# Kernel tuning notes

Hardware: AMD Instinct MI355X
Metric: run time of the kernel (lower is better)

The kernel has to match this reference:

```python
import jax, jax.numpy as jnp
import numpy as np

EPS = 1e-8
L_CENTER, L_ALIGN, L_MARGIN = 1.0, 0.1, 0.05
B, D = 16384, 2048


def setup_inputs() -> dict:
    key = jax.random.key(0)
    kf, kl, ks = jax.random.split(key, 3)
    feats = jax.random.normal(kf, (B, D), dtype=jnp.float32)
    feats = feats / jnp.linalg.norm(feats, axis=-1, keepdims=True)  # module assumes normalized
    labels = jax.random.randint(kl, (B,), 0, 2, dtype=jnp.int32)
    sessions = jax.random.randint(ks, (B,), 0, 2, dtype=jnp.int32)
    return {"features": feats, "labels": labels, "sessions": sessions}


def _cos(a, b):
    # F.cosine_similarity semantics: dot / max(|a||b|, eps)
    num = jnp.sum(a * b, axis=-1)
    den = jnp.maximum(jnp.linalg.norm(a, axis=-1) * jnp.linalg.norm(b, axis=-1), EPS)
    return num / den


def reference(features, labels, sessions):
    # group id: (label, session) -> 2*label + session ; centers order (0,0),(0,1),(1,0),(1,1)
    g = labels * 2 + sessions
    counts = jax.ops.segment_sum(jnp.ones((features.shape[0],), features.dtype), g, num_segments=4)
    sums = jax.ops.segment_sum(features, g, num_segments=4)  # (4, D)
    centers = sums / counts[:, None]

    # 1) center loss: mean over samples of (1 - cos(f_i, center_{g_i}))
    center_loss = jnp.mean(1.0 - _cos(features, centers[g]))

    # 2) align loss: same class, across sessions -> pairs (c00,c01), (c10,c11)
    align_loss = ((1.0 - _cos(centers[0], centers[1])) + (1.0 - _cos(centers[2], centers[3]))) / 2.0

    # 3) angular margin: cross-class center pairs (2x2 = 4 pairs), mean cosine
    c0 = centers[:2]  # class 0 centers (2, D)
    c1 = centers[2:]  # class 1 centers (2, D)
    margin_loss = jnp.mean(_cos(c0[:, None, :], c1[None, :, :]))

    total = L_CENTER * center_loss + L_ALIGN * align_loss + L_MARGIN * margin_loss
    return total, center_loss, align_loss, margin_loss
```

## Files before the change

kernel.cpp:

```cpp
#include <hip/hip_runtime.h>
#include <math.h>

constexpr int B_ROWS = 16384;
constexpr int D_COLS = 2048;
constexpr float EPS_F = 1e-8f;

constexpr int NRB = 256;
constexpr int NCS = 8;
constexpr int ROWS_PER_RB = 64;
constexpr int ROWS_PER_H = 16;

constexpr int WS_DOTS = 2048;
constexpr int WS_PART = 16384;

__global__ __launch_bounds__(256, 8) void pass1_partial_sums(
    const float* __restrict__ feat, const int* __restrict__ lab,
    const int* __restrict__ ses, float* __restrict__ ws) {
  const int t = threadIdx.x;
  const int rb = blockIdx.x >> 3;
  const int cs = blockIdx.x & 7;
  const int c = t & 63;
  const int h = t >> 6;
  const int row0 = rb * ROWS_PER_RB;

  __shared__ float4 w[ROWS_PER_RB];
  __shared__ float4 red[16 * 64];

  if (t < ROWS_PER_RB) {
    const int r = row0 + t;
    const int g = lab[r] * 2 + ses[r];
    w[t] = make_float4(g == 0 ? 1.f : 0.f, g == 1 ? 1.f : 0.f,
                       g == 2 ? 1.f : 0.f, g == 3 ? 1.f : 0.f);
  }
  __syncthreads();

  float4 a0 = {0.f, 0.f, 0.f, 0.f};
  float4 a1 = a0, a2 = a0, a3 = a0;

  const float4* fb = (const float4*)feat
      + (size_t)(row0 + h * ROWS_PER_H) * 512 + cs * 64 + c;
  #pragma unroll 4
  for (int r = 0; r < ROWS_PER_H; ++r) {
    const float4 v = fb[(size_t)r * 512];
    const float4 wr = w[h * ROWS_PER_H + r];
    a0.x += v.x * wr.x; a0.y += v.y * wr.x; a0.z += v.z * wr.x; a0.w += v.w * wr.x;
    a1.x += v.x * wr.y; a1.y += v.y * wr.y; a1.z += v.z * wr.y; a1.w += v.w * wr.y;
    a2.x += v.x * wr.z; a2.y += v.y * wr.z; a2.z += v.z * wr.z; a2.w += v.w * wr.z;
    a3.x += v.x * wr.w; a3.y += v.y * wr.w; a3.z += v.z * wr.w; a3.w += v.w * wr.w;
  }

  red[(0 * 4 + h) * 64 + c] = a0;
  red[(1 * 4 + h) * 64 + c] = a1;
  red[(2 * 4 + h) * 64 + c] = a2;
  red[(3 * 4 + h) * 64 + c] = a3;
  __syncthreads();

  {
    const int g = t >> 6;
    float4 acc = red[(g * 4 + 0) * 64 + c];
    #pragma unroll
    for (int hh = 1; hh < 4; ++hh) {
      const float4 v = red[(g * 4 + hh) * 64 + c];
      acc.x += v.x; acc.y += v.y; acc.z += v.z; acc.w += v.w;
    }
    float4* part = (float4*)(ws + WS_PART);
    part[(size_t)rb * 2048 + g * 512 + cs * 64 + c] = acc;
  }

  if (cs == 0 && t == 0) {
    float4 cnt = {0.f, 0.f, 0.f, 0.f};
    #pragma unroll
    for (int r = 0; r < ROWS_PER_RB; ++r) {
      const float4 wr = w[r];
      cnt.x += wr.x; cnt.y += wr.y; cnt.z += wr.z; cnt.w += wr.w;
    }
    ((float4*)ws)[rb] = cnt;
  }
}

__global__ __launch_bounds__(256) void pass2_reduce(float* __restrict__ ws) {
  const int t = threadIdx.x;
  const int pair = t & 15;
  const int chunk = t >> 4;
  const int g = pair >> 2;
  const int cl = pair & 3;
  const int j4 = g * 512 + blockIdx.x * 4 + cl;

  float4 s = {0.f, 0.f, 0.f, 0.f};
  const float4* part = (const float4*)(ws + WS_PART);
  for (int p = chunk; p < NRB; p += 16) {
    const float4 v = part[(size_t)p * 2048 + j4];
    s.x += v.x; s.y += v.y; s.z += v.z; s.w += v.w;
  }

  __shared__ float4 lds[256];
  lds[t] = s;
  __syncthreads();

  __shared__ float4 sg[4][4];
  if (t < 16) {
    float4 acc = lds[t];
    #pragma unroll
    for (int ch = 1; ch < 16; ++ch) {
      const float4 v = lds[ch * 16 + t];
      acc.x += v.x; acc.y += v.y; acc.z += v.z; acc.w += v.w;
    }
    sg[t >> 2][t & 3] = acc;
  }
  __syncthreads();

  if (t == 0) {
    float n0 = 0, n1 = 0, n2 = 0, n3 = 0;
    float d01 = 0, d23 = 0, d02 = 0, d03 = 0, d12 = 0, d13 = 0;
    #pragma unroll
    for (int cl2 = 0; cl2 < 4; ++cl2) {
      const float4 s0 = sg[0][cl2], s1 = sg[1][cl2];
      const float4 s2 = sg[2][cl2], s3 = sg[3][cl2];
      n0 += s0.x*s0.x + s0.y*s0.y + s0.z*s0.z + s0.w*s0.w;
      n1 += s1.x*s1.x + s1.y*s1.y + s1.z*s1.z + s1.w*s1.w;
      n2 += s2.x*s2.x + s2.y*s2.y + s2.z*s2.z + s2.w*s2.w;
      n3 += s3.x*s3.x + s3.y*s3.y + s3.z*s3.z + s3.w*s3.w;
      d01 += s0.x*s1.x + s0.y*s1.y + s0.z*s1.z + s0.w*s1.w;
      d23 += s2.x*s3.x + s2.y*s3.y + s2.z*s3.z + s2.w*s3.w;
      d02 += s0.x*s2.x + s0.y*s2.y + s0.z*s2.z + s0.w*s2.w;
      d03 += s0.x*s3.x + s0.y*s3.y + s0.z*s3.z + s0.w*s3.w;
      d12 += s1.x*s2.x + s1.y*s2.y + s1.z*s2.z + s1.w*s2.w;
      d13 += s1.x*s3.x + s1.y*s3.y + s1.z*s3.z + s1.w*s3.w;
    }
    float* dst = ws + WS_DOTS + blockIdx.x * 12;
    dst[0] = n0;  dst[1] = n1;  dst[2] = n2;  dst[3] = n3;
    dst[4] = d01; dst[5] = d23; dst[6] = d02; dst[7] = d03;
    dst[8] = d12; dst[9] = d13; dst[10] = 0.f; dst[11] = 0.f;
  }
}

__global__ __launch_bounds__(256) void pass3_finalize(
    const float* __restrict__ ws, float* __restrict__ out) {
  const int t = threadIdx.x;
  float n0 = 0, n1 = 0, n2 = 0, n3 = 0;
  float d01 = 0, d23 = 0, d02 = 0, d03 = 0, d12 = 0, d13 = 0;
  float k0 = 0, k1 = 0, k2 = 0, k3 = 0;

  if (t < 128) {
    const float* src = ws + WS_DOTS + t * 12;
    n0 = src[0]; n1 = src[1]; n2 = src[2]; n3 = src[3];
    d01 = src[4]; d23 = src[5]; d02 = src[6]; d03 = src[7];
    d12 = src[8]; d13 = src[9];
  }
  {
    const float4 cta = ((const float4*)ws)[t];
    k0 = cta.x; k1 = cta.y; k2 = cta.z; k3 = cta.w;
  }

  #pragma unroll
  for (int m = 32; m >= 1; m >>= 1) {
    n0  += __shfl_xor(n0, m, 64);  n1  += __shfl_xor(n1, m, 64);
    n2  += __shfl_xor(n2, m, 64);  n3  += __shfl_xor(n3, m, 64);
    d01 += __shfl_xor(d01, m, 64); d23 += __shfl_xor(d23, m, 64);
    d02 += __shfl_xor(d02, m, 64); d03 += __shfl_xor(d03, m, 64);
    d12 += __shfl_xor(d12, m, 64); d13 += __shfl_xor(d13, m, 64);
    k0  += __shfl_xor(k0, m, 64);  k1  += __shfl_xor(k1, m, 64);
    k2  += __shfl_xor(k2, m, 64);  k3  += __shfl_xor(k3, m, 64);
  }

  __shared__ float red[4][14];
  const int wv = t >> 6, ln = t & 63;
  if (ln == 0) {
    red[wv][0] = n0;  red[wv][1] = n1;  red[wv][2] = n2;  red[wv][3] = n3;
    red[wv][4] = d01; red[wv][5] = d23; red[wv][6] = d02; red[wv][7] = d03;
    red[wv][8] = d12; red[wv][9] = d13;
    red[wv][10] = k0; red[wv][11] = k1; red[wv][12] = k2; red[wv][13] = k3;
  }
  __syncthreads();

  if (t == 0) {
    float v[14];
    #pragma unroll
    for (int k = 0; k < 14; ++k)
      v[k] = red[0][k] + red[1][k] + red[2][k] + red[3][k];

    const float NS0 = sqrtf(v[0]), NS1 = sqrtf(v[1]);
    const float NS2 = sqrtf(v[2]), NS3 = sqrtf(v[3]);
    const float cn0 = v[10], cn1 = v[11], cn2 = v[12], cn3 = v[13];
    const float N0 = NS0 / cn0, N1 = NS1 / cn1;
    const float N2 = NS2 / cn2, N3 = NS3 / cn3;

    const float c01 = (v[4] / (cn0 * cn1)) / fmaxf(N0 * N1, EPS_F);
    const float c23 = (v[5] / (cn2 * cn3)) / fmaxf(N2 * N3, EPS_F);
    const float c02 = (v[6] / (cn0 * cn2)) / fmaxf(N0 * N2, EPS_F);
    const float c03 = (v[7] / (cn0 * cn3)) / fmaxf(N0 * N3, EPS_F);
    const float c12 = (v[8] / (cn1 * cn2)) / fmaxf(N1 * N2, EPS_F);
    const float c13 = (v[9] / (cn1 * cn3)) / fmaxf(N1 * N3, EPS_F);

    const float center_loss = 1.0f - (NS0 + NS1 + NS2 + NS3) * (1.0f / (float)B_ROWS);
    const float align_loss = ((1.0f - c01) + (1.0f - c23)) * 0.5f;
    const float margin_loss = (c02 + c03 + c12 + c13) * 0.25f;

    out[0] = center_loss + 0.1f * align_loss + 0.05f * margin_loss;
    out[1] = center_loss;
    out[2] = align_loss;
    out[3] = margin_loss;
  }
}

extern "C" void kernel_launch(void* const* d_in, const int* in_sizes, int n_in,
                              void* d_out, int out_size, void* d_ws, size_t ws_size,
                              hipStream_t stream) {
  const float* feat = (const float*)d_in[0];
  const int* lab = (const int*)d_in[1];
  const int* ses = (const int*)d_in[2];
  float* ws = (float*)d_ws;
  float* out = (float*)d_out;

  hipLaunchKernelGGL(pass1_partial_sums, dim3(NRB * NCS), dim3(256), 0, stream,
                     feat, lab, ses, ws);
  hipLaunchKernelGGL(pass2_reduce, dim3(128), dim3(256), 0, stream, ws);
  hipLaunchKernelGGL(pass3_finalize, dim3(1), dim3(256), 0, stream, ws, out);
}
```

Measured before the change: 36.44 us.

## Fuse reduce and finalize kernels using a last-block atomic counter

Merges the second-stage reduction and the single-block finalize into one kernel. Each block publishes its partial dot products, then bumps a global atomic counter, and the last block to arrive performs the final reduction and writes the losses. The counter is reset by pass1, so no extra launch is needed. Pass2's grid is doubled to 256 blocks, each handling half as many columns, to spread the partial-sum reads. This drops one kernel launch and its inter-kernel gap, at the cost of threadfences and an atomic per block.

Result: slower. 40.84 us (+12.1%).

```diff
diff --git a/kernel.cpp b/kernel.cpp
--- a/kernel.cpp
+++ b/kernel.cpp
@@ -9,8 +9,10 @@
 constexpr int NCS = 8;
 constexpr int ROWS_PER_RB = 64;
 constexpr int ROWS_PER_H = 16;
+constexpr int NB2 = 256;
 
 constexpr int WS_DOTS = 2048;
+constexpr int CNT_IDX = 8000;
 constexpr int WS_PART = 16384;
 
 __global__ __launch_bounds__(256, 8) void pass1_partial_sums(
@@ -22,6 +24,8 @@
   const int c = t & 63;
   const int h = t >> 6;
   const int row0 = rb * ROWS_PER_RB;
+
+  if (blockIdx.x == 0 && t == 0) ((int*)ws)[CNT_IDX] = 0;
 
   __shared__ float4 w[ROWS_PER_RB];
   __shared__ float4 red[16 * 64];
@@ -78,17 +82,20 @@
   }
 }
 
-__global__ __launch_bounds__(256) void pass2_reduce(float* __restrict__ ws) {
+__global__ __launch_bounds__(256) void pass2_finalize(
+    float* __restrict__ ws, float* __restrict__ out) {
   const int t = threadIdx.x;
-  const int pair = t & 15;
-  const int chunk = t >> 4;
-  const int g = pair >> 2;
-  const int cl = pair & 3;
-  const int j4 = g * 512 + blockIdx.x * 4 + cl;
+  const int b = blockIdx.x;
+  const int pair = t & 7;
+  const int chunk = t >> 3;
+  const int g = pair >> 1;
+  const int cl = pair & 1;
+  const int j4 = g * 512 + b * 2 + cl;
 
   float4 s = {0.f, 0.f, 0.f, 0.f};
   const float4* part = (const float4*)(ws + WS_PART);
-  for (int p = chunk; p < NRB; p += 16) {
+  #pragma unroll
+  for (int p = chunk; p < NRB; p += 32) {
     const float4 v = part[(size_t)p * 2048 + j4];
     s.x += v.x; s.y += v.y; s.z += v.z; s.w += v.w;
   }
@@ -97,23 +104,24 @@
   lds[t] = s;
   __syncthreads();
 
-  __shared__ float4 sg[4][4];
-  if (t < 16) {
+  __shared__ float4 sg[4][2];
+  if (t < 8) {
     float4 acc = lds[t];
     #pragma unroll
-    for (int ch = 1; ch < 16; ++ch) {
-      const float4 v = lds[ch * 16 + t];
+    for (int ch = 1; ch < 32; ++ch) {
+      const float4 v = lds[ch * 8 + t];
       acc.x += v.x; acc.y += v.y; acc.z += v.z; acc.w += v.w;
     }
-    sg[t >> 2][t & 3] = acc;
-  }
-  __syncthreads();
-
+    sg[t >> 1][t & 1] = acc;
+  }
+  __syncthreads();
+
+  __shared__ int lastFlag;
   if (t == 0) {
     float n0 = 0, n1 = 0, n2 = 0, n3 = 0;
     float d01 = 0, d23 = 0, d02 = 0, d03 = 0, d12 = 0, d13 = 0;
     #pragma unroll
-    for (int cl2 = 0; cl2 < 4; ++cl2) {
+    for (int cl2 = 0; cl2 < 2; ++cl2) {
       const float4 s0 = sg[0][cl2], s1 = sg[1][cl2];
       const float4 s2 = sg[2][cl2], s3 = sg[3][cl2];
       n0 += s0.x*s0.x + s0.y*s0.y + s0.z*s0.z + s0.w*s0.w;
@@ -127,27 +135,27 @@
       d12 += s1.x*s2.x + s1.y*s2.y + s1.z*s2.z + s1.w*s2.w;
       d13 += s1.x*s3.x + s1.y*s3.y + s1.z*s3.z + s1.w*s3.w;
     }
-    float* dst = ws + WS_DOTS + blockIdx.x * 12;
+    float* dst = ws + WS_DOTS + b * 12;
     dst[0] = n0;  dst[1] = n1;  dst[2] = n2;  dst[3] = n3;
     dst[4] = d01; dst[5] = d23; dst[6] = d02; dst[7] = d03;
     dst[8] = d12; dst[9] = d13; dst[10] = 0.f; dst[11] = 0.f;
-  }
-}
-
-__global__ __launch_bounds__(256) void pass3_finalize(
-    const float* __restrict__ ws, float* __restrict__ out) {
-  const int t = threadIdx.x;
+
+    __threadfence();
+    const int old = atomicAdd((int*)ws + CNT_IDX, 1);
+    lastFlag = (old == NB2 - 1);
+  }
+  __syncthreads();
+  if (!lastFlag) return;
+  __threadfence();
+
   float n0 = 0, n1 = 0, n2 = 0, n3 = 0;
   float d01 = 0, d23 = 0, d02 = 0, d03 = 0, d12 = 0, d13 = 0;
   float k0 = 0, k1 = 0, k2 = 0, k3 = 0;
-
-  if (t < 128) {
+  {
     const float* src = ws + WS_DOTS + t * 12;
     n0 = src[0]; n1 = src[1]; n2 = src[2]; n3 = src[3];
     d01 = src[4]; d23 = src[5]; d02 = src[6]; d03 = src[7];
     d12 = src[8]; d13 = src[9];
-  }
-  {
     const float4 cta = ((const float4*)ws)[t];
     k0 = cta.x; k1 = cta.y; k2 = cta.z; k3 = cta.w;
   }
@@ -163,13 +171,13 @@
     k2  += __shfl_xor(k2, m, 64);  k3  += __shfl_xor(k3, m, 64);
   }
 
-  __shared__ float red[4][14];
+  __shared__ float red2[4][14];
   const int wv = t >> 6, ln = t & 63;
   if (ln == 0) {
-    red[wv][0] = n0;  red[wv][1] = n1;  red[wv][2] = n2;  red[wv][3] = n3;
-    red[wv][4] = d01; red[wv][5] = d23; red[wv][6] = d02; red[wv][7] = d03;
-    red[wv][8] = d12; red[wv][9] = d13;
-    red[wv][10] = k0; red[wv][11] = k1; red[wv][12] = k2; red[wv][13] = k3;
+    red2[wv][0] = n0;  red2[wv][1] = n1;  red2[wv][2] = n2;  red2[wv][3] = n3;
+    red2[wv][4] = d01; red2[wv][5] = d23; red2[wv][6] = d02; red2[wv][7] = d03;
+    red2[wv][8] = d12; red2[wv][9] = d13;
+    red2[wv][10] = k0; red2[wv][11] = k1; red2[wv][12] = k2; red2[wv][13] = k3;
   }
   __syncthreads();
 
@@ -177,7 +185,7 @@
     float v[14];
     #pragma unroll
     for (int k = 0; k < 14; ++k)
-      v[k] = red[0][k] + red[1][k] + red[2][k] + red[3][k];
+      v[k] = red2[0][k] + red2[1][k] + red2[2][k] + red2[3][k];
 
     const float NS0 = sqrtf(v[0]), NS1 = sqrtf(v[1]);
     const float NS2 = sqrtf(v[2]), NS3 = sqrtf(v[3]);
@@ -214,6 +222,5 @@
 
   hipLaunchKernelGGL(pass1_partial_sums, dim3(NRB * NCS), dim3(256), 0, stream,
                      feat, lab, ses, ws);
-  hipLaunchKernelGGL(pass2_reduce, dim3(128), dim3(256), 0, stream, ws);
-  hipLaunchKernelGGL(pass3_finalize, dim3(1), dim3(256), 0, stream, ws, out);
+  hipLaunchKernelGGL(pass2_finalize, dim3(NB2), dim3(256), 0, stream, ws, out);
 }
```

## Halve row blocks in partial-sum pass and move center dot products to finalize

Applied to the files above, without the earlier changes.

Pass 1 now uses 128-row blocks split into 16 column slices with 8 row groups per block. This halves the partial-sum workspace that pass 2 must read. Pass 2 now only produces the full per-group column sums over 256 blocks, and pass 3 computes all norms and cross dot products from those sums in a single block. The aim is less intermediate memory traffic and a shorter serial single-thread section in pass 2. In exchange, the single-block finalize kernel has to read 32 KB of center sums.

Result: faster. 32.22 us (-11.6%).

```diff
diff --git a/kernel.cpp b/kernel.cpp
--- a/kernel.cpp
+++ b/kernel.cpp
@@ -5,26 +5,27 @@
 constexpr int D_COLS = 2048;
 constexpr float EPS_F = 1e-8f;
 
-constexpr int NRB = 256;
-constexpr int NCS = 8;
-constexpr int ROWS_PER_RB = 64;
-constexpr int ROWS_PER_H = 16;
-
-constexpr int WS_DOTS = 2048;
+constexpr int NRB = 128;
+constexpr int NCS = 16;
+constexpr int ROWS_PER_RB = 128;
+constexpr int NH = 8;
+constexpr int NB2 = 256;
+
+constexpr int WS_CSUM = 2048;
 constexpr int WS_PART = 16384;
 
 __global__ __launch_bounds__(256, 8) void pass1_partial_sums(
     const float* __restrict__ feat, const int* __restrict__ lab,
     const int* __restrict__ ses, float* __restrict__ ws) {
   const int t = threadIdx.x;
-  const int rb = blockIdx.x >> 3;
-  const int cs = blockIdx.x & 7;
-  const int c = t & 63;
-  const int h = t >> 6;
+  const int rb = blockIdx.x >> 4;
+  const int cs = blockIdx.x & 15;
+  const int c = t & 31;
+  const int h = t >> 5;
   const int row0 = rb * ROWS_PER_RB;
 
   __shared__ float4 w[ROWS_PER_RB];
-  __shared__ float4 red[16 * 64];
+  __shared__ float4 red[4 * NH * 32];
 
   if (t < ROWS_PER_RB) {
     const int r = row0 + t;
@@ -38,33 +39,34 @@
   float4 a1 = a0, a2 = a0, a3 = a0;
 
   const float4* fb = (const float4*)feat
-      + (size_t)(row0 + h * ROWS_PER_H) * 512 + cs * 64 + c;
+      + (size_t)(row0 + h * 16) * 512 + cs * 32 + c;
   #pragma unroll 4
-  for (int r = 0; r < ROWS_PER_H; ++r) {
+  for (int r = 0; r < 16; ++r) {
     const float4 v = fb[(size_t)r * 512];
-    const float4 wr = w[h * ROWS_PER_H + r];
+    const float4 wr = w[h * 16 + r];
     a0.x += v.x * wr.x; a0.y += v.y * wr.x; a0.z += v.z * wr.x; a0.w += v.w * wr.x;
     a1.x += v.x * wr.y; a1.y += v.y * wr.y; a1.z += v.z * wr.y; a1.w += v.w * wr.y;
     a2.x += v.x * wr.z; a2.y += v.y * wr.z; a2.z += v.z * wr.z; a2.w += v.w * wr.z;
     a3.x += v.x * wr.w; a3.y += v.y * wr.w; a3.z += v.z * wr.w; a3.w += v.w * wr.w;
   }
 
-  red[(0 * 4 + h) * 64 + c] = a0;
-  red[(1 * 4 + h) * 64 + c] = a1;
-  red[(2 * 4 + h) * 64 + c] = a2;
-  red[(3 * 4 + h) * 64 + c] = a3;
-  __syncthreads();
-
-  {
-    const int g = t >> 6;
-    float4 acc = red[(g * 4 + 0) * 64 + c];
-    #pragma unroll
-    for (int hh = 1; hh < 4; ++hh) {
-      const float4 v = red[(g * 4 + hh) * 64 + c];
+  red[(0 * NH + h) * 32 + c] = a0;
+  red[(1 * NH + h) * 32 + c] = a1;
+  red[(2 * NH + h) * 32 + c] = a2;
+  red[(3 * NH + h) * 32 + c] = a3;
+  __syncthreads();
+
+  if (t < 128) {
+    const int g = t >> 5;
+    const int cc = t & 31;
+    float4 acc = red[(g * NH + 0) * 32 + cc];
+    #pragma unroll
+    for (int hh = 1; hh < NH; ++hh) {
+      const float4 v = red[(g * NH + hh) * 32 + cc];
       acc.x += v.x; acc.y += v.y; acc.z += v.z; acc.w += v.w;
     }
     float4* part = (float4*)(ws + WS_PART);
-    part[(size_t)rb * 2048 + g * 512 + cs * 64 + c] = acc;
+    part[(size_t)rb * 2048 + g * 512 + cs * 32 + cc] = acc;
   }
 
   if (cs == 0 && t == 0) {
@@ -80,15 +82,15 @@
 
 __global__ __launch_bounds__(256) void pass2_reduce(float* __restrict__ ws) {
   const int t = threadIdx.x;
-  const int pair = t & 15;
-  const int chunk = t >> 4;
-  const int g = pair >> 2;
-  const int cl = pair & 3;
-  const int j4 = g * 512 + blockIdx.x * 4 + cl;
+  const int b = blockIdx.x;
+  const int cl = t & 7;
+  const int chunk = t >> 3;
+  const int j4 = b * 8 + cl;
 
   float4 s = {0.f, 0.f, 0.f, 0.f};
   const float4* part = (const float4*)(ws + WS_PART);
-  for (int p = chunk; p < NRB; p += 16) {
+  #pragma unroll
+  for (int p = chunk; p < NRB; p += 32) {
     const float4 v = part[(size_t)p * 2048 + j4];
     s.x += v.x; s.y += v.y; s.z += v.z; s.w += v.w;
   }
@@ -97,57 +99,44 @@
   lds[t] = s;
   __syncthreads();
 
-  __shared__ float4 sg[4][4];
-  if (t < 16) {
+  if (t < 8) {
     float4 acc = lds[t];
     #pragma unroll
-    for (int ch = 1; ch < 16; ++ch) {
-      const float4 v = lds[ch * 16 + t];
+    for (int ch = 1; ch < 32; ++ch) {
+      const float4 v = lds[ch * 8 + t];
       acc.x += v.x; acc.y += v.y; acc.z += v.z; acc.w += v.w;
     }
-    sg[t >> 2][t & 3] = acc;
-  }
-  __syncthreads();
-
-  if (t == 0) {
-    float n0 = 0, n1 = 0, n2 = 0, n3 = 0;
-    float d01 = 0, d23 = 0, d02 = 0, d03 = 0, d12 = 0, d13 = 0;
-    #pragma unroll
-    for (int cl2 = 0; cl2 < 4; ++cl2) {
-      const float4 s0 = sg[0][cl2], s1 = sg[1][cl2];
-      const float4 s2 = sg[2][cl2], s3 = sg[3][cl2];
-      n0 += s0.x*s0.x + s0.y*s0.y + s0.z*s0.z + s0.w*s0.w;
-      n1 += s1.x*s1.x + s1.y*s1.y + s1.z*s1.z + s1.w*s1.w;
-      n2 += s2.x*s2.x + s2.y*s2.y + s2.z*s2.z + s2.w*s2.w;
-      n3 += s3.x*s3.x + s3.y*s3.y + s3.z*s3.z + s3.w*s3.w;
-      d01 += s0.x*s1.x + s0.y*s1.y + s0.z*s1.z + s0.w*s1.w;
-      d23 += s2.x*s3.x + s2.y*s3.y + s2.z*s3.z + s2.w*s3.w;
-      d02 += s0.x*s2.x + s0.y*s2.y + s0.z*s2.z + s0.w*s2.w;
-      d03 += s0.x*s3.x + s0.y*s3.y + s0.z*s3.z + s0.w*s3.w;
-      d12 += s1.x*s2.x + s1.y*s2.y + s1.z*s2.z + s1.w*s2.w;
-      d13 += s1.x*s3.x + s1.y*s3.y + s1.z*s3.z + s1.w*s3.w;
-    }
-    float* dst = ws + WS_DOTS + blockIdx.x * 12;
-    dst[0] = n0;  dst[1] = n1;  dst[2] = n2;  dst[3] = n3;
-    dst[4] = d01; dst[5] = d23; dst[6] = d02; dst[7] = d03;
-    dst[8] = d12; dst[9] = d13; dst[10] = 0.f; dst[11] = 0.f;
+    ((float4*)(ws + WS_CSUM))[b * 8 + t] = acc;
   }
 }
 
 __global__ __launch_bounds__(256) void pass3_finalize(
     const float* __restrict__ ws, float* __restrict__ out) {
   const int t = threadIdx.x;
+  const float4* csum = (const float4*)(ws + WS_CSUM);
   float n0 = 0, n1 = 0, n2 = 0, n3 = 0;
   float d01 = 0, d23 = 0, d02 = 0, d03 = 0, d12 = 0, d13 = 0;
   float k0 = 0, k1 = 0, k2 = 0, k3 = 0;
 
-  if (t < 128) {
-    const float* src = ws + WS_DOTS + t * 12;
-    n0 = src[0]; n1 = src[1]; n2 = src[2]; n3 = src[3];
-    d01 = src[4]; d23 = src[5]; d02 = src[6]; d03 = src[7];
-    d12 = src[8]; d13 = src[9];
-  }
-  {
+  #pragma unroll
+  for (int jj = 0; jj < 2; ++jj) {
+    const int j = t + jj * 256;
+    const float4 s0 = csum[j];
+    const float4 s1 = csum[512 + j];
+    const float4 s2 = csum[1024 + j];
+    const float4 s3 = csum[1536 + j];
+    n0 += s0.x*s0.x + s0.y*s0.y + s0.z*s0.z + s0.w*s0.w;
+    n1 += s1.x*s1.x + s1.y*s1.y + s1.z*s1.z + s1.w*s1.w;
+    n2 += s2.x*s2.x + s2.y*s2.y + s2.z*s2.z + s2.w*s2.w;
+    n3 += s3.x*s3.x + s3.y*s3.y + s3.z*s3.z + s3.w*s3.w;
+    d01 += s0.x*s1.x + s0.y*s1.y + s0.z*s1.z + s0.w*s1.w;
+    d23 += s2.x*s3.x + s2.y*s3.y + s2.z*s3.z + s2.w*s3.w;
+    d02 += s0.x*s2.x + s0.y*s2.y + s0.z*s2.z + s0.w*s2.w;
+    d03 += s0.x*s3.x + s0.y*s3.y + s0.z*s3.z + s0.w*s3.w;
+    d12 += s1.x*s2.x + s1.y*s2.y + s1.z*s2.z + s1.w*s2.w;
+    d13 += s1.x*s3.x + s1.y*s3.y + s1.z*s3.z + s1.w*s3.w;
+  }
+  if (t < NRB) {
     const float4 cta = ((const float4*)ws)[t];
     k0 = cta.x; k1 = cta.y; k2 = cta.z; k3 = cta.w;
   }
@@ -214,6 +203,6 @@
 
   hipLaunchKernelGGL(pass1_partial_sums, dim3(NRB * NCS), dim3(256), 0, stream,
                      feat, lab, ses, ws);
-  hipLaunchKernelGGL(pass2_reduce, dim3(128), dim3(256), 0, stream, ws);
+  hipLaunchKernelGGL(pass2_reduce, dim3(NB2), dim3(256), 0, stream, ws);
   hipLaunchKernelGGL(pass3_finalize, dim3(1), dim3(256), 0, stream, ws, out);
 }
```
